# Optimization experiments

Hardware: AMD Instinct MI355X
Metric: run time of the kernel (lower is better)

Reference implementation:

```python
import jax, jax.numpy as jnp
import numpy as np

HEADS = 16
HEAD_DIM = 64
HIDDEN = HEADS * HEAD_DIM  # 1024
COMPRESSION = 1.0  # concat([o, p], -1) forces compressed seq len == T, i.e. scale 1
LN_EPS = 1e-5


def _interp_linear_seq(x, scale):
    # F.interpolate(mode='linear', align_corners=False) along the sequence axis.
    # x: [B, T, C] -> [B, int(T*scale), C]
    T = x.shape[1]
    S = int(T * scale)
    src = (jnp.arange(S, dtype=jnp.float32) + 0.5) / scale - 0.5
    src = jnp.clip(src, 0.0, T - 1)
    lo = jnp.floor(src).astype(jnp.int32)
    hi = jnp.minimum(lo + 1, T - 1)
    w = (src - lo.astype(jnp.float32))[None, :, None]
    return x[:, lo] * (1.0 - w) + x[:, hi] * w


def _rotary(x):
    # rotate-half rotary embedding; x: [B, S, h, d]
    S, d = x.shape[1], x.shape[3]
    inv_freq = 1.0 / (10000.0 ** (jnp.arange(0, d, 2, dtype=jnp.float32) / d))
    ang = jnp.arange(S, dtype=jnp.float32)[:, None] * inv_freq  # [S, d/2]
    cos = jnp.cos(ang)[None, :, None, :]
    sin = jnp.sin(ang)[None, :, None, :]
    x1, x2 = jnp.split(x, 2, axis=-1)
    return jnp.concatenate([x1 * cos - x2 * sin, x1 * sin + x2 * cos], axis=-1)


def setup_inputs() -> dict:
    key = jax.random.key(0)
    ks = jax.random.split(key, 4)
    B, T = 4, 2048
    x = jax.random.normal(ks[0], (B, T, HIDDEN), dtype=jnp.float32)
    ln_gamma = jnp.ones((HIDDEN,), dtype=jnp.float32)
    ln_beta = jnp.zeros((HIDDEN,), dtype=jnp.float32)
    w_in = jax.random.normal(ks[1], (HIDDEN, 7 * HIDDEN), dtype=jnp.float32) * (HIDDEN ** -0.5)
    w_out = jax.random.normal(ks[2], (5 * HIDDEN, HIDDEN), dtype=jnp.float32) * ((5 * HIDDEN) ** -0.5)
    b_out = jnp.zeros((HIDDEN,), dtype=jnp.float32)
    return {"x": x, "ln_gamma": ln_gamma, "ln_beta": ln_beta,
            "w_in": w_in, "w_out": w_out, "b_out": b_out}


def reference(x, ln_gamma, ln_beta, w_in, w_out, b_out):
    B, T, _ = x.shape
    # LayerNorm
    mu = jnp.mean(x, axis=-1, keepdims=True)
    var = jnp.mean(jnp.square(x - mu), axis=-1, keepdims=True)
    xn = (x - mu) / jnp.sqrt(var + LN_EPS) * ln_gamma + ln_beta
    # fused QKVP projection (no bias)
    qkvp = xn @ w_in  # [B, T, 7*HIDDEN]
    q, k, v, p = jnp.split(qkvp, [HIDDEN, 2 * HIDDEN, 3 * HIDDEN], axis=-1)
    # linear-interpolation compression of k, v, p along the sequence axis
    k = _interp_linear_seq(k, COMPRESSION)
    v = _interp_linear_seq(v, COMPRESSION)
    p = _interp_linear_seq(p, COMPRESSION)
    S = k.shape[1]
    q = q.reshape(B, T, HEADS, HEAD_DIM)
    k = k.reshape(B, S, HEADS, HEAD_DIM)
    v = v.reshape(B, S, HEADS, HEAD_DIM)
    q = _rotary(q)
    k = _rotary(k)
    # manual softmax attention (no mask in the original)
    a = jnp.einsum('bihd,bjhd->bhij', q, k) * (HEAD_DIM ** -0.5)
    a = jax.nn.softmax(a, axis=-1)
    o = jnp.einsum('bhij,bjhd->bihd', a, v).reshape(B, T, HIDDEN)
    # GELU side branch (torch F.gelu default = exact erf gelu)
    p = jax.nn.gelu(p, approximate=False)
    return jnp.concatenate([o, p], axis=-1) @ w_out + b_out
```

## Files before the change

kernel.cpp:

```cpp
#include <hip/hip_runtime.h>
#include <hip/hip_bf16.h>
#include <math.h>

typedef short bf16x8 __attribute__((ext_vector_type(8)));
typedef float f32x4 __attribute__((ext_vector_type(4)));

#define HEADS 16
#define HDIM 64
#define HID 1024
#define B_ 4
#define T_ 2048
#define BT_ (B_*T_)
#define N1 (7*HID)
#define K2 (5*HID)

#define SM_SCALE_LOG2E 0.18033688011111793f

__device__ __forceinline__ float bf2f(unsigned short u) {
  union { unsigned int i; float f; } c; c.i = ((unsigned int)u) << 16; return c.f;
}
__device__ __forceinline__ unsigned short f2bf(float f) {
  __hip_bfloat16 h = __float2bfloat16(f);
  return __builtin_bit_cast(unsigned short, h);
}
__device__ __forceinline__ unsigned int cvt_pk_bf16(float a, float b) {
  unsigned int r;
  asm("v_cvt_pk_bf16_f32 %0, %1, %2" : "=v"(r) : "v"(a), "v"(b));
  return r;
}
__device__ __forceinline__ float gelu_fast(float x) {
  float y = 0.7978845608028654f * (x + 0.044715f * x * x * x);
  float e = exp2f(y * 2.8853900817779268f);
  float t = 1.f - 2.f / (e + 1.f);
  return 0.5f * x * (1.f + t);
}

__global__ __launch_bounds__(256) void tcast_kernel(const float* __restrict__ in,
                                                    unsigned short* __restrict__ out,
                                                    int R, int C) {
  __shared__ float tile[64][65];
  int tx = threadIdx.x & 63;
  int ty = threadIdx.x >> 6;
  long r0 = (long)blockIdx.y * 64;
  long c0 = (long)blockIdx.x * 64;
#pragma unroll
  for (int i = 0; i < 16; i++) {
    int r = ty + i * 4;
    tile[r][tx] = in[(r0 + r) * C + c0 + tx];
  }
  __syncthreads();
#pragma unroll
  for (int i = 0; i < 16; i++) {
    int rr = ty + i * 4;
    out[(c0 + rr) * R + r0 + tx] = f2bf(tile[tx][rr]);
  }
}

__global__ __launch_bounds__(256) void ln_kernel(const float* __restrict__ x,
                                                 const float* __restrict__ g,
                                                 const float* __restrict__ b,
                                                 unsigned short* __restrict__ xn) {
  int row = blockIdx.x, tid = threadIdx.x;
  float4 v = reinterpret_cast<const float4*>(x + (long)row * HID)[tid];
  float s = v.x + v.y + v.z + v.w;
  float sq = v.x * v.x + v.y * v.y + v.z * v.z + v.w * v.w;
#pragma unroll
  for (int off = 32; off > 0; off >>= 1) { s += __shfl_down(s, off); sq += __shfl_down(sq, off); }
  __shared__ float red[8];
  int wid = tid >> 6, lane = tid & 63;
  if (lane == 0) { red[wid] = s; red[4 + wid] = sq; }
  __syncthreads();
  if (tid == 0) {
    red[0] = red[0] + red[1] + red[2] + red[3];
    red[4] = red[4] + red[5] + red[6] + red[7];
  }
  __syncthreads();
  float mean = red[0] * (1.f / HID);
  float var  = red[4] * (1.f / HID) - mean * mean;
  float rstd = rsqrtf(var + 1e-5f);
  float4 gv = reinterpret_cast<const float4*>(g)[tid];
  float4 bv = reinterpret_cast<const float4*>(b)[tid];
  ushort4 o;
  o.x = f2bf((v.x - mean) * rstd * gv.x + bv.x);
  o.y = f2bf((v.y - mean) * rstd * gv.y + bv.y);
  o.z = f2bf((v.z - mean) * rstd * gv.z + bv.z);
  o.w = f2bf((v.w - mean) * rstd * gv.w + bv.w);
  reinterpret_cast<ushort4*>(xn + (long)row * HID)[tid] = o;
}

__device__ __forceinline__ void gemm_core_db(const unsigned short* __restrict__ A,
                                             const unsigned short* __restrict__ BT,
                                             unsigned short* As, unsigned short* Bs,
                                             int K, int lda, int ldb,
                                             long row0, long col0,
                                             int lane, int wid, f32x4 (&acc)[4][4]) {
  int l15 = lane & 15, lq = lane >> 4;
  int srow = lane >> 2;
  int schnk = lane & 3;
  int r0s = wid * 32 + srow;
  int r1s = r0s + 16;
  int slot0 = schnk ^ ((r0s >> 1) & 3);
  int slot1 = schnk ^ ((r1s >> 1) & 3);
  const unsigned short* a0 = A + (row0 + r0s) * (long)lda + schnk * 8;
  const unsigned short* a1 = A + (row0 + r1s) * (long)lda + schnk * 8;
  const unsigned short* b0 = BT + (col0 + r0s) * (long)ldb + schnk * 8;
  const unsigned short* b1 = BT + (col0 + r1s) * (long)ldb + schnk * 8;
  int wm = (wid & 1) * 64, wn = (wid >> 1) * 64;
  int NT = K / 32;

  bf16x8 ar0 = *reinterpret_cast<const bf16x8*>(a0);
  bf16x8 ar1 = *reinterpret_cast<const bf16x8*>(a1);
  bf16x8 br0 = *reinterpret_cast<const bf16x8*>(b0);
  bf16x8 br1 = *reinterpret_cast<const bf16x8*>(b1);
  *reinterpret_cast<bf16x8*>(&As[r0s * 32 + slot0 * 8]) = ar0;
  *reinterpret_cast<bf16x8*>(&As[r1s * 32 + slot1 * 8]) = ar1;
  *reinterpret_cast<bf16x8*>(&Bs[r0s * 32 + slot0 * 8]) = br0;
  *reinterpret_cast<bf16x8*>(&Bs[r1s * 32 + slot1 * 8]) = br1;
  ar0 = *reinterpret_cast<const bf16x8*>(a0 + 32);
  ar1 = *reinterpret_cast<const bf16x8*>(a1 + 32);
  br0 = *reinterpret_cast<const bf16x8*>(b0 + 32);
  br1 = *reinterpret_cast<const bf16x8*>(b1 + 32);
  __syncthreads();

  int cur = 0;
  for (int t = 0; t < NT; t++) {
    const unsigned short* Asr = As + cur * 4096;
    const unsigned short* Bsr = Bs + cur * 4096;
    bf16x8 af[4], bfv[4];
#pragma unroll
    for (int m = 0; m < 4; m++) {
      int r = wm + m * 16 + l15;
      af[m] = *reinterpret_cast<const bf16x8*>(&Asr[r * 32 + (lq ^ ((r >> 1) & 3)) * 8]);
    }
#pragma unroll
    for (int n = 0; n < 4; n++) {
      int r = wn + n * 16 + l15;
      bfv[n] = *reinterpret_cast<const bf16x8*>(&Bsr[r * 32 + (lq ^ ((r >> 1) & 3)) * 8]);
    }
    if (t + 1 < NT) {
      unsigned short* Asw = As + (cur ^ 1) * 4096;
      unsigned short* Bsw = Bs + (cur ^ 1) * 4096;
      *reinterpret_cast<bf16x8*>(&Asw[r0s * 32 + slot0 * 8]) = ar0;
      *reinterpret_cast<bf16x8*>(&Asw[r1s * 32 + slot1 * 8]) = ar1;
      *reinterpret_cast<bf16x8*>(&Bsw[r0s * 32 + slot0 * 8]) = br0;
      *reinterpret_cast<bf16x8*>(&Bsw[r1s * 32 + slot1 * 8]) = br1;
    }
    if (t + 2 < NT) {
      long ko = (long)(t + 2) * 32;
      ar0 = *reinterpret_cast<const bf16x8*>(a0 + ko);
      ar1 = *reinterpret_cast<const bf16x8*>(a1 + ko);
      br0 = *reinterpret_cast<const bf16x8*>(b0 + ko);
      br1 = *reinterpret_cast<const bf16x8*>(b1 + ko);
    }
#pragma unroll
    for (int m = 0; m < 4; m++)
#pragma unroll
      for (int n = 0; n < 4; n++)
        acc[m][n] = __builtin_amdgcn_mfma_f32_16x16x32_bf16(af[m], bfv[n], acc[m][n], 0, 0, 0);
    __syncthreads();
    cur ^= 1;
  }
}

__global__ __launch_bounds__(256) void gemm1_fused(const unsigned short* __restrict__ A,
                                                   const unsigned short* __restrict__ BT,
                                                   unsigned short* __restrict__ q_r,
                                                   unsigned short* __restrict__ k_r,
                                                   unsigned short* __restrict__ v_t,
                                                   unsigned short* __restrict__ C5) {
  __shared__ unsigned short smem[18432];
  unsigned short* As = smem;
  unsigned short* Bs = smem + 8192;
  int tid = threadIdx.x, lane = tid & 63, wid = tid >> 6;
  long row0 = (long)blockIdx.y * 128;
  long col0 = (long)blockIdx.x * 128;
  f32x4 acc[4][4] = {};
  gemm_core_db(A, BT, As, Bs, HID, HID, HID, row0, col0, lane, wid, acc);

  int wm = (wid & 1) * 64, wn = (wid >> 1) * 64;
  long row_base = row0 + wm;
  int b = (int)(row_base >> 11);
  int t_base = (int)(row_base & 2047);
  int col_base = (int)col0 + wn;
  int region = col_base >> 10;
  int l15 = lane & 15, lq = lane >> 4;

  if (region <= 1) {
    unsigned short* dst = (region == 0) ? q_r : k_r;
    float osc = (region == 0) ? SM_SCALE_LOG2E : 1.0f;
    int head = (col_base & 1023) >> 6;
    long obase = (long)(b * 16 + head) * T_ * 64;
    float fr[2];
    fr[0] = __expf(-(float)l15 * 0.28782313662425572f);
    fr[1] = __expf(-(float)(16 + l15) * 0.28782313662425572f);
#pragma unroll
    for (int m = 0; m < 4; m++) {
#pragma unroll
      for (int j = 0; j < 4; j++) {
        int t = t_base + m * 16 + lq * 4 + j;
#pragma unroll
        for (int n = 0; n < 2; n++) {
          float sn, cs;
          __sincosf((float)t * fr[n], &sn, &cs);
          float xl = acc[m][n][j], xh = acc[m][n + 2][j];
          int d = n * 16 + l15;
          dst[obase + (long)t * 64 + d]      = f2bf((xl * cs - xh * sn) * osc);
          dst[obase + (long)t * 64 + d + 32] = f2bf((xl * sn + xh * cs) * osc);
        }
      }
    }
  } else if (region == 2) {
    int head = (col_base & 1023) >> 6;
    unsigned short* vt = smem + wid * 4608;
#pragma unroll
    for (int m = 0; m < 4; m++)
#pragma unroll
      for (int n = 0; n < 4; n++)
#pragma unroll
        for (int j = 0; j < 4; j++)
          vt[(n * 16 + l15) * 72 + m * 16 + lq * 4 + j] = f2bf(acc[m][n][j]);
    long obase = (long)(b * 16 + head) * 64 * T_;
#pragma unroll
    for (int i = 0; i < 8; i++) {
      int d = i * 8 + (lane >> 3);
      int tl = (lane & 7) * 8;
      bf16x8 v = *reinterpret_cast<const bf16x8*>(&vt[d * 72 + tl]);
      *reinterpret_cast<bf16x8*>(v_t + obase + (long)d * T_ + t_base + tl) = v;
    }
  } else {
    int colp = col_base - 3 * HID;
#pragma unroll
    for (int m = 0; m < 4; m++) {
#pragma unroll
      for (int j = 0; j < 4; j++) {
        long row = row_base + m * 16 + lq * 4 + j;
#pragma unroll
        for (int n = 0; n < 4; n++)
          C5[row * K2 + HID + colp + n * 16 + l15] = f2bf(gelu_fast(acc[m][n][j]));
      }
    }
  }
}

__global__ __launch_bounds__(256) void gemm_bt(const unsigned short* __restrict__ A,
                                               const unsigned short* __restrict__ BT,
                                               float* __restrict__ Cout,
                                               const float* __restrict__ bias,
                                               int K, int lda, int ldb, int ldc) {
  __shared__ unsigned short smem[16384];
  unsigned short* As = smem;
  unsigned short* Bs = smem + 8192;
  int tid = threadIdx.x, lane = tid & 63, wid = tid >> 6;
  long row0 = (long)blockIdx.y * 128;
  long col0 = (long)blockIdx.x * 128;
  f32x4 acc[4][4] = {};
  gemm_core_db(A, BT, As, Bs, K, lda, ldb, row0, col0, lane, wid, acc);
  int wm = (wid & 1) * 64, wn = (wid >> 1) * 64;
#pragma unroll
  for (int m = 0; m < 4; m++) {
#pragma unroll
    for (int n = 0; n < 4; n++) {
      long r = row0 + wm + m * 16 + (lane >> 4) * 4;
      long c = col0 + wn + n * 16 + (lane & 15);
#pragma unroll
      for (int j = 0; j < 4; j++)
        Cout[(r + j) * (long)ldc + c] = acc[m][n][j] + bias[c];
    }
  }
}

__global__ __launch_bounds__(256) void attn_kernel(const unsigned short* __restrict__ q_r,
                                                   const unsigned short* __restrict__ k_r,
                                                   const unsigned short* __restrict__ v_t,
                                                   unsigned short* __restrict__ C5) {
  int qt = blockIdx.x;
  int bh = blockIdx.y;
  int b = bh >> 4, h = bh & 15;
  int tid = threadIdx.x, lane = tid & 63, wid = tid >> 6;
  int l15 = lane & 15, lq = lane >> 4;
  __shared__ unsigned short Ks[64 * 64];
  __shared__ unsigned short Vts[64 * 64];
  __shared__ unsigned short Ps[4][32 * 64];

  const unsigned short* qbase = q_r + ((long)bh * T_ + qt * 128 + wid * 32) * 64;
  bf16x8 aq[2][2];
#pragma unroll
  for (int m = 0; m < 2; m++)
#pragma unroll
    for (int kk = 0; kk < 2; kk++)
      aq[m][kk] = *reinterpret_cast<const bf16x8*>(
          qbase + (m * 16 + l15) * 64 + kk * 32 + lq * 8);

  f32x4 o_acc[2][4] = {};
  float l_run[2] = {0.f, 0.f};

  const unsigned short* kbase = k_r + (long)bh * T_ * 64;
  const unsigned short* vbase = v_t + (long)bh * 64 * T_;
  int srow = lane >> 3;
  int schnk = lane & 7;
  int slot = schnk ^ srow;
  unsigned short* Pw = &Ps[wid][0];

  bf16x8 kreg[2], vreg[2];
#pragma unroll
  for (int i = 0; i < 2; i++) {
    int c = wid * 2 + i;
    kreg[i] = *reinterpret_cast<const bf16x8*>(kbase + c * 512 + lane * 8);
    vreg[i] = *reinterpret_cast<const bf16x8*>(vbase + (long)(c * 8 + srow) * T_ + schnk * 8);
  }

  for (int kt = 0; kt < 32; kt++) {
#pragma unroll
    for (int i = 0; i < 2; i++) {
      int r = (wid * 2 + i) * 8 + srow;
      *reinterpret_cast<bf16x8*>(&Ks[r * 64 + slot * 8])  = kreg[i];
      *reinterpret_cast<bf16x8*>(&Vts[r * 64 + slot * 8]) = vreg[i];
    }
    if (kt < 31) {
#pragma unroll
      for (int i = 0; i < 2; i++) {
        int c = wid * 2 + i;
        kreg[i] = *reinterpret_cast<const bf16x8*>(kbase + (kt + 1) * 4096 + c * 512 + lane * 8);
        vreg[i] = *reinterpret_cast<const bf16x8*>(vbase + (long)(c * 8 + srow) * T_ + (kt + 1) * 64 + schnk * 8);
      }
    }
    __syncthreads();
    f32x4 s2[4][2] = {};
#pragma unroll
    for (int n = 0; n < 4; n++) {
      int krow = n * 16 + l15;
      bf16x8 kf[2];
#pragma unroll
      for (int kk = 0; kk < 2; kk++)
        kf[kk] = *reinterpret_cast<const bf16x8*>(
            &Ks[krow * 64 + ((kk * 4 + lq) ^ (krow & 7)) * 8]);
#pragma unroll
      for (int m = 0; m < 2; m++)
#pragma unroll
        for (int kk = 0; kk < 2; kk++)
          s2[n][m] = __builtin_amdgcn_mfma_f32_16x16x32_bf16(kf[kk], aq[m][kk], s2[n][m], 0, 0, 0);
    }
#pragma unroll
    for (int m = 0; m < 2; m++) {
      unsigned short* prow = Pw + (m * 16 + l15) * 64;
#pragma unroll
      for (int n = 0; n < 4; n++) {
        float p0 = exp2f(s2[n][m][0]);
        float p1 = exp2f(s2[n][m][1]);
        float p2 = exp2f(s2[n][m][2]);
        float p3 = exp2f(s2[n][m][3]);
        l_run[m] += (p0 + p1) + (p2 + p3);
        unsigned int lo = cvt_pk_bf16(p0, p1);
        unsigned int hi = cvt_pk_bf16(p2, p3);
        int cc = (n * 2 + (lq >> 1)) ^ (l15 & 7);
        uint2 w; w.x = lo; w.y = hi;
        *reinterpret_cast<uint2*>(prow + cc * 8 + (lq & 1) * 4) = w;
      }
    }
    bf16x8 ap[2][2];
#pragma unroll
    for (int m = 0; m < 2; m++)
#pragma unroll
      for (int kk = 0; kk < 2; kk++) {
        int cr = (kk * 4 + lq) ^ (l15 & 7);
        ap[m][kk] = *reinterpret_cast<const bf16x8*>(&Pw[(m * 16 + l15) * 64 + cr * 8]);
      }
#pragma unroll
    for (int n = 0; n < 4; n++) {
      int vrow = n * 16 + l15;
      bf16x8 bv[2];
#pragma unroll
      for (int kk = 0; kk < 2; kk++)
        bv[kk] = *reinterpret_cast<const bf16x8*>(
            &Vts[vrow * 64 + ((kk * 4 + lq) ^ (vrow & 7)) * 8]);
#pragma unroll
      for (int m = 0; m < 2; m++)
#pragma unroll
        for (int kk = 0; kk < 2; kk++)
          o_acc[m][n] = __builtin_amdgcn_mfma_f32_16x16x32_bf16(ap[m][kk], bv[kk], o_acc[m][n], 0, 0, 0);
    }
    __syncthreads();
  }
#pragma unroll
  for (int m = 0; m < 2; m++) {
    float l = l_run[m];
    l += __shfl_xor(l, 16);
    l += __shfl_xor(l, 32);
    l_run[m] = l;
  }
#pragma unroll
  for (int m = 0; m < 2; m++)
#pragma unroll
    for (int j = 0; j < 4; j++) {
      float lsum = __shfl(l_run[m], lq * 4 + j);
      float inv = 1.0f / lsum;
      int tl = qt * 128 + wid * 32 + m * 16 + lq * 4 + j;
      long row = (long)b * T_ + tl;
#pragma unroll
      for (int n = 0; n < 4; n++) {
        int col = h * 64 + n * 16 + l15;
        C5[row * K2 + col] = f2bf(o_acc[m][n][j] * inv);
      }
    }
}

extern "C" void kernel_launch(void* const* d_in, const int* in_sizes, int n_in,
                              void* d_out, int out_size, void* d_ws, size_t ws_size,
                              hipStream_t stream) {
  const float* x     = (const float*)d_in[0];
  const float* g     = (const float*)d_in[1];
  const float* be    = (const float*)d_in[2];
  const float* w_in  = (const float*)d_in[3];
  const float* w_out = (const float*)d_in[4];
  const float* b_out = (const float*)d_in[5];
  float* out = (float*)d_out;

  char* ws = (char*)d_ws;
  size_t off = 0;
  auto alloc = [&](size_t bytes) {
    void* p = ws + off;
    off += (bytes + 255) & ~(size_t)255;
    return p;
  };
  unsigned short* xn     = (unsigned short*)alloc((size_t)BT_ * HID * 2);
  unsigned short* w_inT  = (unsigned short*)alloc((size_t)N1 * HID * 2);
  unsigned short* w_outT = (unsigned short*)alloc((size_t)HID * K2 * 2);
  unsigned short* q_rb   = (unsigned short*)alloc((size_t)BT_ * HID * 2);
  unsigned short* k_rb   = (unsigned short*)alloc((size_t)BT_ * HID * 2);
  unsigned short* v_tb   = (unsigned short*)alloc((size_t)BT_ * HID * 2);
  unsigned short* C5     = (unsigned short*)alloc((size_t)BT_ * K2 * 2);

  tcast_kernel<<<dim3(N1 / 64, HID / 64), 256, 0, stream>>>(w_in, w_inT, HID, N1);
  tcast_kernel<<<dim3(HID / 64, K2 / 64), 256, 0, stream>>>(w_out, w_outT, K2, HID);
  ln_kernel<<<BT_, 256, 0, stream>>>(x, g, be, xn);
  gemm1_fused<<<dim3(N1 / 128, BT_ / 128), 256, 0, stream>>>(xn, w_inT, q_rb, k_rb, v_tb, C5);
  attn_kernel<<<dim3(T_ / 128, 64), 256, 0, stream>>>(q_rb, k_rb, v_tb, C5);
  gemm_bt<<<dim3(HID / 128, BT_ / 128), 256, 0, stream>>>(C5, w_outT, out, b_out,
                                                          K2, K2, K2, HID);
}
```

Baseline: 414.2 us.

## Enlarge QKVP projection GEMM tile to 256x256 with 8 waves

```diff
diff --git a/kernel.cpp b/kernel.cpp
--- a/kernel.cpp
+++ b/kernel.cpp
@@ -86,6 +86,145 @@
   o.z = f2bf((v.z - mean) * rstd * gv.z + bv.z);
   o.w = f2bf((v.w - mean) * rstd * gv.w + bv.w);
   reinterpret_cast<ushort4*>(xn + (long)row * HID)[tid] = o;
+}
+
+__global__ __launch_bounds__(512) void gemm1_fused(const unsigned short* __restrict__ A,
+                                                   const unsigned short* __restrict__ BT,
+                                                   unsigned short* __restrict__ q_r,
+                                                   unsigned short* __restrict__ k_r,
+                                                   unsigned short* __restrict__ v_t,
+                                                   unsigned short* __restrict__ C5) {
+  extern __shared__ unsigned short smem[];
+  unsigned short* As = smem;
+  unsigned short* Bs = smem + 16384;
+  int tid = threadIdx.x, lane = tid & 63, wid = tid >> 6;
+  int l15 = lane & 15, lq = lane >> 4;
+  int wr = wid >> 2, wc = wid & 3;
+  long row0 = (long)blockIdx.y * 256;
+  long col0 = (long)blockIdx.x * 256;
+  f32x4 acc[8][4] = {};
+
+  int sr0 = tid >> 2;
+  int sr1 = sr0 + 128;
+  int sch = tid & 3;
+  int sl0 = sch ^ ((sr0 >> 1) & 3);
+  int sl1 = sch ^ ((sr1 >> 1) & 3);
+  const unsigned short* a0 = A + (row0 + sr0) * (long)HID + sch * 8;
+  const unsigned short* a1 = A + (row0 + sr1) * (long)HID + sch * 8;
+  const unsigned short* b0 = BT + (col0 + sr0) * (long)HID + sch * 8;
+  const unsigned short* b1 = BT + (col0 + sr1) * (long)HID + sch * 8;
+
+  bf16x8 ar0 = *reinterpret_cast<const bf16x8*>(a0);
+  bf16x8 ar1 = *reinterpret_cast<const bf16x8*>(a1);
+  bf16x8 br0 = *reinterpret_cast<const bf16x8*>(b0);
+  bf16x8 br1 = *reinterpret_cast<const bf16x8*>(b1);
+  *reinterpret_cast<bf16x8*>(&As[sr0 * 32 + sl0 * 8]) = ar0;
+  *reinterpret_cast<bf16x8*>(&As[sr1 * 32 + sl1 * 8]) = ar1;
+  *reinterpret_cast<bf16x8*>(&Bs[sr0 * 32 + sl0 * 8]) = br0;
+  *reinterpret_cast<bf16x8*>(&Bs[sr1 * 32 + sl1 * 8]) = br1;
+  ar0 = *reinterpret_cast<const bf16x8*>(a0 + 32);
+  ar1 = *reinterpret_cast<const bf16x8*>(a1 + 32);
+  br0 = *reinterpret_cast<const bf16x8*>(b0 + 32);
+  br1 = *reinterpret_cast<const bf16x8*>(b1 + 32);
+  __syncthreads();
+
+  const int NT = HID / 32;
+  int cur = 0;
+  for (int t = 0; t < NT; t++) {
+    const unsigned short* Asr = As + cur * 8192;
+    const unsigned short* Bsr = Bs + cur * 8192;
+    bf16x8 af[8], bfv[4];
+#pragma unroll
+    for (int m = 0; m < 8; m++) {
+      int r = wr * 128 + m * 16 + l15;
+      af[m] = *reinterpret_cast<const bf16x8*>(&Asr[r * 32 + (lq ^ ((r >> 1) & 3)) * 8]);
+    }
+#pragma unroll
+    for (int n = 0; n < 4; n++) {
+      int r = wc * 64 + n * 16 + l15;
+      bfv[n] = *reinterpret_cast<const bf16x8*>(&Bsr[r * 32 + (lq ^ ((r >> 1) & 3)) * 8]);
+    }
+    if (t + 1 < NT) {
+      unsigned short* Asw = As + (cur ^ 1) * 8192;
+      unsigned short* Bsw = Bs + (cur ^ 1) * 8192;
+      *reinterpret_cast<bf16x8*>(&Asw[sr0 * 32 + sl0 * 8]) = ar0;
+      *reinterpret_cast<bf16x8*>(&Asw[sr1 * 32 + sl1 * 8]) = ar1;
+      *reinterpret_cast<bf16x8*>(&Bsw[sr0 * 32 + sl0 * 8]) = br0;
+      *reinterpret_cast<bf16x8*>(&Bsw[sr1 * 32 + sl1 * 8]) = br1;
+    }
+    if (t + 2 < NT) {
+      long ko = (long)(t + 2) * 32;
+      ar0 = *reinterpret_cast<const bf16x8*>(a0 + ko);
+      ar1 = *reinterpret_cast<const bf16x8*>(a1 + ko);
+      br0 = *reinterpret_cast<const bf16x8*>(b0 + ko);
+      br1 = *reinterpret_cast<const bf16x8*>(b1 + ko);
+    }
+#pragma unroll
+    for (int m = 0; m < 8; m++)
+#pragma unroll
+      for (int n = 0; n < 4; n++)
+        acc[m][n] = __builtin_amdgcn_mfma_f32_16x16x32_bf16(af[m], bfv[n], acc[m][n], 0, 0, 0);
+    __syncthreads();
+    cur ^= 1;
+  }
+
+  long row_w = row0 + wr * 128;
+  int b = (int)(row_w >> 11);
+  int t_base = (int)(row_w & 2047);
+  int col_w = (int)col0 + wc * 64;
+  int region = col_w >> 10;
+  int head = (col_w & 1023) >> 6;
+
+  if (region <= 1) {
+    unsigned short* dst = (region == 0) ? q_r : k_r;
+    float osc = (region == 0) ? SM_SCALE_LOG2E : 1.0f;
+    long obase = (long)(b * 16 + head) * T_ * 64;
+    float fr[2];
+    fr[0] = __expf(-(float)l15 * 0.28782313662425572f);
+    fr[1] = __expf(-(float)(16 + l15) * 0.28782313662425572f);
+#pragma unroll
+    for (int m = 0; m < 8; m++) {
+#pragma unroll
+      for (int j = 0; j < 4; j++) {
+        int t = t_base + m * 16 + lq * 4 + j;
+#pragma unroll
+        for (int n = 0; n < 2; n++) {
+          float sn, cs;
+          __sincosf((float)t * fr[n], &sn, &cs);
+          float xl = acc[m][n][j], xh = acc[m][n + 2][j];
+          int d = n * 16 + l15;
+          dst[obase + (long)t * 64 + d]      = f2bf((xl * cs - xh * sn) * osc);
+          dst[obase + (long)t * 64 + d + 32] = f2bf((xl * sn + xh * cs) * osc);
+        }
+      }
+    }
+  } else if (region == 2) {
+    long obase = (long)(b * 16 + head) * 64 * T_;
+#pragma unroll
+    for (int m = 0; m < 8; m++) {
+      int t0 = t_base + m * 16 + lq * 4;
+#pragma unroll
+      for (int n = 0; n < 4; n++) {
+        int d = n * 16 + l15;
+        uint2 w;
+        w.x = cvt_pk_bf16(acc[m][n][0], acc[m][n][1]);
+        w.y = cvt_pk_bf16(acc[m][n][2], acc[m][n][3]);
+        *reinterpret_cast<uint2*>(v_t + obase + (long)d * T_ + t0) = w;
+      }
+    }
+  } else {
+    int colp = col_w - 3 * HID;
+#pragma unroll
+    for (int m = 0; m < 8; m++) {
+#pragma unroll
+      for (int j = 0; j < 4; j++) {
+        long row = row_w + m * 16 + lq * 4 + j;
+#pragma unroll
+        for (int n = 0; n < 4; n++)
+          C5[row * K2 + HID + colp + n * 16 + l15] = f2bf(gelu_fast(acc[m][n][j]));
+      }
+    }
+  }
 }
 
 __device__ __forceinline__ void gemm_core_db(const unsigned short* __restrict__ A,
@@ -162,94 +301,14 @@
   }
 }
 
-__global__ __launch_bounds__(256) void gemm1_fused(const unsigned short* __restrict__ A,
-                                                   const unsigned short* __restrict__ BT,
-                                                   unsigned short* __restrict__ q_r,
-                                                   unsigned short* __restrict__ k_r,
-                                                   unsigned short* __restrict__ v_t,
-                                                   unsigned short* __restrict__ C5) {
-  __shared__ unsigned short smem[18432];
-  unsigned short* As = smem;
-  unsigned short* Bs = smem + 8192;
-  int tid = threadIdx.x, lane = tid & 63, wid = tid >> 6;
-  long row0 = (long)blockIdx.y * 128;
-  long col0 = (long)blockIdx.x * 128;
-  f32x4 acc[4][4] = {};
-  gemm_core_db(A, BT, As, Bs, HID, HID, HID, row0, col0, lane, wid, acc);
-
-  int wm = (wid & 1) * 64, wn = (wid >> 1) * 64;
-  long row_base = row0 + wm;
-  int b = (int)(row_base >> 11);
-  int t_base = (int)(row_base & 2047);
-  int col_base = (int)col0 + wn;
-  int region = col_base >> 10;
-  int l15 = lane & 15, lq = lane >> 4;
-
-  if (region <= 1) {
-    unsigned short* dst = (region == 0) ? q_r : k_r;
-    float osc = (region == 0) ? SM_SCALE_LOG2E : 1.0f;
-    int head = (col_base & 1023) >> 6;
-    long obase = (long)(b * 16 + head) * T_ * 64;
-    float fr[2];
-    fr[0] = __expf(-(float)l15 * 0.28782313662425572f);
-    fr[1] = __expf(-(float)(16 + l15) * 0.28782313662425572f);
-#pragma unroll
-    for (int m = 0; m < 4; m++) {
-#pragma unroll
-      for (int j = 0; j < 4; j++) {
-        int t = t_base + m * 16 + lq * 4 + j;
-#pragma unroll
-        for (int n = 0; n < 2; n++) {
-          float sn, cs;
-          __sincosf((float)t * fr[n], &sn, &cs);
-          float xl = acc[m][n][j], xh = acc[m][n + 2][j];
-          int d = n * 16 + l15;
-          dst[obase + (long)t * 64 + d]      = f2bf((xl * cs - xh * sn) * osc);
-          dst[obase + (long)t * 64 + d + 32] = f2bf((xl * sn + xh * cs) * osc);
-        }
-      }
-    }
-  } else if (region == 2) {
-    int head = (col_base & 1023) >> 6;
-    unsigned short* vt = smem + wid * 4608;
-#pragma unroll
-    for (int m = 0; m < 4; m++)
-#pragma unroll
-      for (int n = 0; n < 4; n++)
-#pragma unroll
-        for (int j = 0; j < 4; j++)
-          vt[(n * 16 + l15) * 72 + m * 16 + lq * 4 + j] = f2bf(acc[m][n][j]);
-    long obase = (long)(b * 16 + head) * 64 * T_;
-#pragma unroll
-    for (int i = 0; i < 8; i++) {
-      int d = i * 8 + (lane >> 3);
-      int tl = (lane & 7) * 8;
-      bf16x8 v = *reinterpret_cast<const bf16x8*>(&vt[d * 72 + tl]);
-      *reinterpret_cast<bf16x8*>(v_t + obase + (long)d * T_ + t_base + tl) = v;
-    }
-  } else {
-    int colp = col_base - 3 * HID;
-#pragma unroll
-    for (int m = 0; m < 4; m++) {
-#pragma unroll
-      for (int j = 0; j < 4; j++) {
-        long row = row_base + m * 16 + lq * 4 + j;
-#pragma unroll
-        for (int n = 0; n < 4; n++)
-          C5[row * K2 + HID + colp + n * 16 + l15] = f2bf(gelu_fast(acc[m][n][j]));
-      }
-    }
-  }
-}
-
 __global__ __launch_bounds__(256) void gemm_bt(const unsigned short* __restrict__ A,
                                                const unsigned short* __restrict__ BT,
                                                float* __restrict__ Cout,
                                                const float* __restrict__ bias,
                                                int K, int lda, int ldb, int ldc) {
-  __shared__ unsigned short smem[16384];
-  unsigned short* As = smem;
-  unsigned short* Bs = smem + 8192;
+  __shared__ unsigned short smem2[16384];
+  unsigned short* As = smem2;
+  unsigned short* Bs = smem2 + 8192;
   int tid = threadIdx.x, lane = tid & 63, wid = tid >> 6;
   long row0 = (long)blockIdx.y * 128;
   long col0 = (long)blockIdx.x * 128;
@@ -433,7 +492,7 @@
   tcast_kernel<<<dim3(N1 / 64, HID / 64), 256, 0, stream>>>(w_in, w_inT, HID, N1);
   tcast_kernel<<<dim3(HID / 64, K2 / 64), 256, 0, stream>>>(w_out, w_outT, K2, HID);
   ln_kernel<<<BT_, 256, 0, stream>>>(x, g, be, xn);
-  gemm1_fused<<<dim3(N1 / 128, BT_ / 128), 256, 0, stream>>>(xn, w_inT, q_rb, k_rb, v_tb, C5);
+  gemm1_fused<<<dim3(N1 / 256, BT_ / 256), 512, 65536, stream>>>(xn, w_inT, q_rb, k_rb, v_tb, C5);
   attn_kernel<<<dim3(T_ / 128, 64), 256, 0, stream>>>(q_rb, k_rb, v_tb, C5);
   gemm_bt<<<dim3(HID / 128, BT_ / 128), 256, 0, stream>>>(C5, w_outT, out, b_out,
                                                           K2, K2, K2, HID);
```

New measurement: 420.6 us. About the same (+1.5%).

## Double-buffer K/V tiles in attention and use 512-thread blocks over 256 queries

Applied to the files above, without the earlier changes.

```diff
diff --git a/kernel.cpp b/kernel.cpp
--- a/kernel.cpp
+++ b/kernel.cpp
@@ -247,9 +247,9 @@
                                                float* __restrict__ Cout,
                                                const float* __restrict__ bias,
                                                int K, int lda, int ldb, int ldc) {
-  __shared__ unsigned short smem[16384];
-  unsigned short* As = smem;
-  unsigned short* Bs = smem + 8192;
+  __shared__ unsigned short smem2[16384];
+  unsigned short* As = smem2;
+  unsigned short* Bs = smem2 + 8192;
   int tid = threadIdx.x, lane = tid & 63, wid = tid >> 6;
   long row0 = (long)blockIdx.y * 128;
   long col0 = (long)blockIdx.x * 128;
@@ -269,7 +269,7 @@
   }
 }
 
-__global__ __launch_bounds__(256) void attn_kernel(const unsigned short* __restrict__ q_r,
+__global__ __launch_bounds__(512) void attn_kernel(const unsigned short* __restrict__ q_r,
                                                    const unsigned short* __restrict__ k_r,
                                                    const unsigned short* __restrict__ v_t,
                                                    unsigned short* __restrict__ C5) {
@@ -278,11 +278,12 @@
   int b = bh >> 4, h = bh & 15;
   int tid = threadIdx.x, lane = tid & 63, wid = tid >> 6;
   int l15 = lane & 15, lq = lane >> 4;
-  __shared__ unsigned short Ks[64 * 64];
-  __shared__ unsigned short Vts[64 * 64];
-  __shared__ unsigned short Ps[4][32 * 64];
-
-  const unsigned short* qbase = q_r + ((long)bh * T_ + qt * 128 + wid * 32) * 64;
+  extern __shared__ unsigned short sm[];
+  unsigned short* Ks  = sm;
+  unsigned short* Vts = sm + 8192;
+  unsigned short* Pw  = sm + 16384 + wid * 2048;
+
+  const unsigned short* qbase = q_r + ((long)bh * T_ + qt * 256 + wid * 32) * 64;
   bf16x8 aq[2][2];
 #pragma unroll
   for (int m = 0; m < 2; m++)
@@ -296,35 +297,30 @@
 
   const unsigned short* kbase = k_r + (long)bh * T_ * 64;
   const unsigned short* vbase = v_t + (long)bh * 64 * T_;
-  int srow = lane >> 3;
-  int schnk = lane & 7;
-  int slot = schnk ^ srow;
-  unsigned short* Pw = &Ps[wid][0];
-
-  bf16x8 kreg[2], vreg[2];
-#pragma unroll
-  for (int i = 0; i < 2; i++) {
-    int c = wid * 2 + i;
-    kreg[i] = *reinterpret_cast<const bf16x8*>(kbase + c * 512 + lane * 8);
-    vreg[i] = *reinterpret_cast<const bf16x8*>(vbase + (long)(c * 8 + srow) * T_ + schnk * 8);
-  }
-
+  int srow = tid >> 3;
+  int schnk = tid & 7;
+  int slot = schnk ^ (srow & 7);
+
+  bf16x8 kreg = *reinterpret_cast<const bf16x8*>(kbase + srow * 64 + schnk * 8);
+  bf16x8 vreg = *reinterpret_cast<const bf16x8*>(vbase + (long)srow * T_ + schnk * 8);
+  *reinterpret_cast<bf16x8*>(&Ks[srow * 64 + slot * 8])  = kreg;
+  *reinterpret_cast<bf16x8*>(&Vts[srow * 64 + slot * 8]) = vreg;
+  kreg = *reinterpret_cast<const bf16x8*>(kbase + 4096 + srow * 64 + schnk * 8);
+  vreg = *reinterpret_cast<const bf16x8*>(vbase + (long)srow * T_ + 64 + schnk * 8);
+  __syncthreads();
+
+  int cur = 0;
   for (int kt = 0; kt < 32; kt++) {
-#pragma unroll
-    for (int i = 0; i < 2; i++) {
-      int r = (wid * 2 + i) * 8 + srow;
-      *reinterpret_cast<bf16x8*>(&Ks[r * 64 + slot * 8])  = kreg[i];
-      *reinterpret_cast<bf16x8*>(&Vts[r * 64 + slot * 8]) = vreg[i];
-    }
     if (kt < 31) {
-#pragma unroll
-      for (int i = 0; i < 2; i++) {
-        int c = wid * 2 + i;
-        kreg[i] = *reinterpret_cast<const bf16x8*>(kbase + (kt + 1) * 4096 + c * 512 + lane * 8);
-        vreg[i] = *reinterpret_cast<const bf16x8*>(vbase + (long)(c * 8 + srow) * T_ + (kt + 1) * 64 + schnk * 8);
-      }
-    }
-    __syncthreads();
+      *reinterpret_cast<bf16x8*>(&Ks[(cur ^ 1) * 4096 + srow * 64 + slot * 8])  = kreg;
+      *reinterpret_cast<bf16x8*>(&Vts[(cur ^ 1) * 4096 + srow * 64 + slot * 8]) = vreg;
+    }
+    if (kt < 30) {
+      kreg = *reinterpret_cast<const bf16x8*>(kbase + (kt + 2) * 4096 + srow * 64 + schnk * 8);
+      vreg = *reinterpret_cast<const bf16x8*>(vbase + (long)srow * T_ + (kt + 2) * 64 + schnk * 8);
+    }
+    const unsigned short* Kc = Ks + cur * 4096;
+    const unsigned short* Vc = Vts + cur * 4096;
     f32x4 s2[4][2] = {};
 #pragma unroll
     for (int n = 0; n < 4; n++) {
@@ -333,7 +329,7 @@
 #pragma unroll
       for (int kk = 0; kk < 2; kk++)
         kf[kk] = *reinterpret_cast<const bf16x8*>(
-            &Ks[krow * 64 + ((kk * 4 + lq) ^ (krow & 7)) * 8]);
+            &Kc[krow * 64 + ((kk * 4 + lq) ^ (krow & 7)) * 8]);
 #pragma unroll
       for (int m = 0; m < 2; m++)
 #pragma unroll
@@ -372,7 +368,7 @@
 #pragma unroll
       for (int kk = 0; kk < 2; kk++)
         bv[kk] = *reinterpret_cast<const bf16x8*>(
-            &Vts[vrow * 64 + ((kk * 4 + lq) ^ (vrow & 7)) * 8]);
+            &Vc[vrow * 64 + ((kk * 4 + lq) ^ (vrow & 7)) * 8]);
 #pragma unroll
       for (int m = 0; m < 2; m++)
 #pragma unroll
@@ -380,6 +376,7 @@
           o_acc[m][n] = __builtin_amdgcn_mfma_f32_16x16x32_bf16(ap[m][kk], bv[kk], o_acc[m][n], 0, 0, 0);
     }
     __syncthreads();
+    cur ^= 1;
   }
 #pragma unroll
   for (int m = 0; m < 2; m++) {
@@ -394,7 +391,7 @@
     for (int j = 0; j < 4; j++) {
       float lsum = __shfl(l_run[m], lq * 4 + j);
       float inv = 1.0f / lsum;
-      int tl = qt * 128 + wid * 32 + m * 16 + lq * 4 + j;
+      int tl = qt * 256 + wid * 32 + m * 16 + lq * 4 + j;
       long row = (long)b * T_ + tl;
 #pragma unroll
       for (int n = 0; n < 4; n++) {
@@ -434,7 +431,7 @@
   tcast_kernel<<<dim3(HID / 64, K2 / 64), 256, 0, stream>>>(w_out, w_outT, K2, HID);
   ln_kernel<<<BT_, 256, 0, stream>>>(x, g, be, xn);
   gemm1_fused<<<dim3(N1 / 128, BT_ / 128), 256, 0, stream>>>(xn, w_inT, q_rb, k_rb, v_tb, C5);
-  attn_kernel<<<dim3(T_ / 128, 64), 256, 0, stream>>>(q_rb, k_rb, v_tb, C5);
+  attn_kernel<<<dim3(T_ / 256, 64), 512, 65536, stream>>>(q_rb, k_rb, v_tb, C5);
   gemm_bt<<<dim3(HID / 128, BT_ / 128), 256, 0, stream>>>(C5, w_outT, out, b_out,
                                                           K2, K2, K2, HID);
 }
```

Measured after the change: 422.0 us. No clear change (+1.9%).

## Stream GEMM tiles into LDS with direct global-to-LDS async loads

Applied to the files above, without the earlier changes.

```diff
diff --git a/kernel.cpp b/kernel.cpp
--- a/kernel.cpp
+++ b/kernel.cpp
@@ -33,6 +33,12 @@
   float e = exp2f(y * 2.8853900817779268f);
   float t = 1.f - 2.f / (e + 1.f);
   return 0.5f * x * (1.f + t);
+}
+
+typedef __attribute__((address_space(1))) const unsigned int gu32;
+typedef __attribute__((address_space(3))) unsigned int lu32;
+__device__ __forceinline__ void async16(const void* g, void* l) {
+  __builtin_amdgcn_global_load_lds((gu32*)g, (lu32*)l, 16, 0, 0);
 }
 
 __global__ __launch_bounds__(256) void tcast_kernel(const float* __restrict__ in,
@@ -88,42 +94,39 @@
   reinterpret_cast<ushort4*>(xn + (long)row * HID)[tid] = o;
 }
 
-__device__ __forceinline__ void gemm_core_db(const unsigned short* __restrict__ A,
-                                             const unsigned short* __restrict__ BT,
-                                             unsigned short* As, unsigned short* Bs,
-                                             int K, int lda, int ldb,
-                                             long row0, long col0,
-                                             int lane, int wid, f32x4 (&acc)[4][4]) {
+__device__ __forceinline__ void gemm_core_dma(const unsigned short* __restrict__ A,
+                                              const unsigned short* __restrict__ BT,
+                                              unsigned short* As, unsigned short* Bs,
+                                              int K, int lda, int ldb,
+                                              long row0, long col0,
+                                              int lane, int wid, f32x4 (&acc)[4][4]) {
   int l15 = lane & 15, lq = lane >> 4;
-  int srow = lane >> 2;
-  int schnk = lane & 3;
-  int r0s = wid * 32 + srow;
-  int r1s = r0s + 16;
-  int slot0 = schnk ^ ((r0s >> 1) & 3);
-  int slot1 = schnk ^ ((r1s >> 1) & 3);
-  const unsigned short* a0 = A + (row0 + r0s) * (long)lda + schnk * 8;
-  const unsigned short* a1 = A + (row0 + r1s) * (long)lda + schnk * 8;
-  const unsigned short* b0 = BT + (col0 + r0s) * (long)ldb + schnk * 8;
-  const unsigned short* b1 = BT + (col0 + r1s) * (long)ldb + schnk * 8;
+  int d  = lane >> 2;
+  int ch = (lane & 3) ^ ((lane >> 3) & 3);
+  int R0 = wid * 32;
+  const unsigned short* aS0 = A + (row0 + R0 + d)      * (long)lda + ch * 8;
+  const unsigned short* aS1 = A + (row0 + R0 + 16 + d) * (long)lda + ch * 8;
+  const unsigned short* bS0 = BT + (col0 + R0 + d)      * (long)ldb + ch * 8;
+  const unsigned short* bS1 = BT + (col0 + R0 + 16 + d) * (long)ldb + ch * 8;
   int wm = (wid & 1) * 64, wn = (wid >> 1) * 64;
   int NT = K / 32;
 
-  bf16x8 ar0 = *reinterpret_cast<const bf16x8*>(a0);
-  bf16x8 ar1 = *reinterpret_cast<const bf16x8*>(a1);
-  bf16x8 br0 = *reinterpret_cast<const bf16x8*>(b0);
-  bf16x8 br1 = *reinterpret_cast<const bf16x8*>(b1);
-  *reinterpret_cast<bf16x8*>(&As[r0s * 32 + slot0 * 8]) = ar0;
-  *reinterpret_cast<bf16x8*>(&As[r1s * 32 + slot1 * 8]) = ar1;
-  *reinterpret_cast<bf16x8*>(&Bs[r0s * 32 + slot0 * 8]) = br0;
-  *reinterpret_cast<bf16x8*>(&Bs[r1s * 32 + slot1 * 8]) = br1;
-  ar0 = *reinterpret_cast<const bf16x8*>(a0 + 32);
-  ar1 = *reinterpret_cast<const bf16x8*>(a1 + 32);
-  br0 = *reinterpret_cast<const bf16x8*>(b0 + 32);
-  br1 = *reinterpret_cast<const bf16x8*>(b1 + 32);
+  async16(aS0, &As[R0 * 32]);
+  async16(aS1, &As[(R0 + 16) * 32]);
+  async16(bS0, &Bs[R0 * 32]);
+  async16(bS1, &Bs[(R0 + 16) * 32]);
   __syncthreads();
 
   int cur = 0;
   for (int t = 0; t < NT; t++) {
+    if (t + 1 < NT) {
+      long ko = (long)(t + 1) * 32;
+      int bo = (cur ^ 1) * 4096;
+      async16(aS0 + ko, &As[bo + R0 * 32]);
+      async16(aS1 + ko, &As[bo + (R0 + 16) * 32]);
+      async16(bS0 + ko, &Bs[bo + R0 * 32]);
+      async16(bS1 + ko, &Bs[bo + (R0 + 16) * 32]);
+    }
     const unsigned short* Asr = As + cur * 4096;
     const unsigned short* Bsr = Bs + cur * 4096;
     bf16x8 af[4], bfv[4];
@@ -136,21 +139,6 @@
     for (int n = 0; n < 4; n++) {
       int r = wn + n * 16 + l15;
       bfv[n] = *reinterpret_cast<const bf16x8*>(&Bsr[r * 32 + (lq ^ ((r >> 1) & 3)) * 8]);
-    }
-    if (t + 1 < NT) {
-      unsigned short* Asw = As + (cur ^ 1) * 4096;
-      unsigned short* Bsw = Bs + (cur ^ 1) * 4096;
-      *reinterpret_cast<bf16x8*>(&Asw[r0s * 32 + slot0 * 8]) = ar0;
-      *reinterpret_cast<bf16x8*>(&Asw[r1s * 32 + slot1 * 8]) = ar1;
-      *reinterpret_cast<bf16x8*>(&Bsw[r0s * 32 + slot0 * 8]) = br0;
-      *reinterpret_cast<bf16x8*>(&Bsw[r1s * 32 + slot1 * 8]) = br1;
-    }
-    if (t + 2 < NT) {
-      long ko = (long)(t + 2) * 32;
-      ar0 = *reinterpret_cast<const bf16x8*>(a0 + ko);
-      ar1 = *reinterpret_cast<const bf16x8*>(a1 + ko);
-      br0 = *reinterpret_cast<const bf16x8*>(b0 + ko);
-      br1 = *reinterpret_cast<const bf16x8*>(b1 + ko);
     }
 #pragma unroll
     for (int m = 0; m < 4; m++)
@@ -175,7 +163,7 @@
   long row0 = (long)blockIdx.y * 128;
   long col0 = (long)blockIdx.x * 128;
   f32x4 acc[4][4] = {};
-  gemm_core_db(A, BT, As, Bs, HID, HID, HID, row0, col0, lane, wid, acc);
+  gemm_core_dma(A, BT, As, Bs, HID, HID, HID, row0, col0, lane, wid, acc);
 
   int wm = (wid & 1) * 64, wn = (wid >> 1) * 64;
   long row_base = row0 + wm;
@@ -203,9 +191,9 @@
           float sn, cs;
           __sincosf((float)t * fr[n], &sn, &cs);
           float xl = acc[m][n][j], xh = acc[m][n + 2][j];
-          int d = n * 16 + l15;
-          dst[obase + (long)t * 64 + d]      = f2bf((xl * cs - xh * sn) * osc);
-          dst[obase + (long)t * 64 + d + 32] = f2bf((xl * sn + xh * cs) * osc);
+          int dd = n * 16 + l15;
+          dst[obase + (long)t * 64 + dd]      = f2bf((xl * cs - xh * sn) * osc);
+          dst[obase + (long)t * 64 + dd + 32] = f2bf((xl * sn + xh * cs) * osc);
         }
       }
     }
@@ -222,10 +210,10 @@
     long obase = (long)(b * 16 + head) * 64 * T_;
 #pragma unroll
     for (int i = 0; i < 8; i++) {
-      int d = i * 8 + (lane >> 3);
+      int dd = i * 8 + (lane >> 3);
       int tl = (lane & 7) * 8;
-      bf16x8 v = *reinterpret_cast<const bf16x8*>(&vt[d * 72 + tl]);
-      *reinterpret_cast<bf16x8*>(v_t + obase + (long)d * T_ + t_base + tl) = v;
+      bf16x8 v = *reinterpret_cast<const bf16x8*>(&vt[dd * 72 + tl]);
+      *reinterpret_cast<bf16x8*>(v_t + obase + (long)dd * T_ + t_base + tl) = v;
     }
   } else {
     int colp = col_base - 3 * HID;
@@ -247,14 +235,14 @@
                                                float* __restrict__ Cout,
                                                const float* __restrict__ bias,
                                                int K, int lda, int ldb, int ldc) {
-  __shared__ unsigned short smem[16384];
-  unsigned short* As = smem;
-  unsigned short* Bs = smem + 8192;
+  __shared__ unsigned short smem2[16384];
+  unsigned short* As = smem2;
+  unsigned short* Bs = smem2 + 8192;
   int tid = threadIdx.x, lane = tid & 63, wid = tid >> 6;
   long row0 = (long)blockIdx.y * 128;
   long col0 = (long)blockIdx.x * 128;
   f32x4 acc[4][4] = {};
-  gemm_core_db(A, BT, As, Bs, K, lda, ldb, row0, col0, lane, wid, acc);
+  gemm_core_dma(A, BT, As, Bs, K, lda, ldb, row0, col0, lane, wid, acc);
   int wm = (wid & 1) * 64, wn = (wid >> 1) * 64;
 #pragma unroll
   for (int m = 0; m < 4; m++) {
```

Measured after the change: 427.1 us. 1.03x slower.
